# Optimization experiments

Hardware: AMD Instinct MI355X
Metric: run time of the kernel (lower is better)

The kernel has to match this reference:

```python
import jax, jax.numpy as jnp
import numpy as np

SAMPLERATE = 22050
N_OCTAVES = 16
N_SAMPLES = 2 ** 15  # 32768
N_EVENTS = 64
BATCH = 4
MIN_HZ = 20
MAX_HZ = 3000
BASE_RESONANCE = 0.01

MIN_FREQ = MIN_HZ / (SAMPLERATE // 2)
MAX_FREQ = MAX_HZ / (SAMPLERATE // 2)
FREQ_RANGE = MAX_FREQ - MIN_FREQ


def setup_inputs() -> dict:
    key = jax.random.key(0)
    k1, k2, k3, k4 = jax.random.split(key, 4)
    return {
        "f0": jax.random.uniform(k1, (BATCH, N_EVENTS, 1), dtype=jnp.float32),
        "decay_coefficients": jax.random.normal(k2, (BATCH, N_EVENTS, 1), dtype=jnp.float32),
        "phase_offsets": jax.random.normal(k3, (BATCH, N_EVENTS, 1), dtype=jnp.float32),
        "freq_spacing": jax.random.uniform(k4, (BATCH, N_EVENTS, 1), dtype=jnp.float32),
    }


def reference(f0, decay_coefficients, phase_offsets, freq_spacing):
    b, e, _ = f0.shape
    f0 = jnp.abs(f0)  # (B, E, 1)

    # computed in the original forward but never used in the output
    _ = jax.nn.sigmoid(phase_offsets) * np.pi

    # exponential_decay(torch.sigmoid(decay_coefficients), ...) -> double sigmoid
    dv = jax.nn.sigmoid(jax.nn.sigmoid(decay_coefficients))  # (B, E, 1)
    resonance_factor = (1.0 - BASE_RESONANCE) * 0.95
    decay = BASE_RESONANCE + dv * resonance_factor
    log_decay = jnp.log(decay + 1e-12)
    # cumsum of the constant over n_frames = n_octaves; F.interpolate to the
    # same size (n_samples=n_octaves in the call) is an identity.
    exp_decays = jnp.exp(jnp.cumsum(
        jnp.broadcast_to(log_decay, (b, e, N_OCTAVES)), axis=-1))  # (B, E, O)

    f0 = (MIN_FREQ + f0 * FREQ_RANGE) * np.pi  # (B, E, 1)
    factors = jnp.cumsum(
        jnp.broadcast_to(freq_spacing, (b, e, N_OCTAVES)), axis=-1)  # (B, E, O)
    f0s = f0 * factors  # (B, E, O) per-octave angular increments

    # cumulative phase over samples, then sin oscillator bank
    phase = jnp.cumsum(
        jnp.broadcast_to(f0s[..., None], (b, e, N_OCTAVES, N_SAMPLES)), axis=-1)
    osc = jnp.sin(phase) * exp_decays[..., None]  # (B, E, O, S)
    osc = jnp.sum(osc, axis=2)  # (B, E, S)

    # max_norm along the sample dim
    mx = jnp.max(jnp.abs(osc), axis=-1, keepdims=True)
    return osc / (mx + 1e-8)
```

## Files before the change

kernel.cpp:

```cpp
#include <hip/hip_runtime.h>
#include <math.h>

#pragma clang fp contract(off)

constexpr int NSAMP = 32768;
constexpr int NROWS = 256;
constexpr int NOCT  = 16;
constexpr int SEGS  = 16;
constexpr int TPB   = 256;
constexpr int GRID  = NROWS * SEGS;

__device__ __forceinline__ float keepf(float x) {
  asm volatile("" : "+v"(x));
  return x;
}

__global__ __launch_bounds__(TPB, 8) void f0res_k1(
    const float* __restrict__ f0_in,
    const float* __restrict__ dec_in,
    const float* __restrict__ fs_in,
    float* __restrict__ out,
    float* __restrict__ segmax)
{
  const int bid = blockIdx.x;
  const int row = bid >> 4;
  const int seg = bid & 15;
  const int t   = threadIdx.x;

  __shared__ float s_tab[NOCT][64];
  __shared__ float s_w[NOCT];
  __shared__ float s_carr[NOCT][128];
  __shared__ float s_red[TPB / 64];

  const float f0a = fabsf(f0_in[row]);
  const float dcc = dec_in[row];
  const float fsv = fs_in[row];

  const float MIN_F = (float)(20.0 / 11025.0);
  const float RNG_F = (float)(3000.0 / 11025.0 - 20.0 / 11025.0);
  const float c1s   = keepf(f0a * RNG_F);
  const float c2s   = keepf(MIN_F + c1s);
  const float f0ang = keepf(c2s * (float)M_PI);

  const float sg    = 1.0f / (1.0f + expf(-dcc));
  const float dvv   = 1.0f / (1.0f + expf(-sg));
  const float dvr   = keepf(dvv * 0.9405f);
  const float decay = keepf(0.01f + dvr);
  const float ldv   = logf(decay + 1e-12f);

  if (t < NOCT) {
    const int k = t;
    float fac = 0.0f;
    for (int j = 0; j <= k; ++j) fac = fac + fsv;
    const float x = keepf(f0ang * fac);
    float* tab = s_tab[k];
    float a = 0.0f;
#pragma unroll
    for (int i = 0; i < 16; ++i) { a = a + x;  tab[i]      = a; }
    const float T0 = a; a = 0.0f;
#pragma unroll
    for (int i = 0; i < 16; ++i) { a = a + T0; tab[16 + i] = a; }
    const float T1 = a; a = 0.0f;
#pragma unroll
    for (int i = 0; i < 16; ++i) { a = a + T1; tab[32 + i] = a; }
    const float T2 = a; a = 0.0f;
#pragma unroll
    for (int i = 0; i < 8;  ++i) { a = a + T2; tab[48 + i] = a; }
    float lc = 0.0f;
    for (int j = 0; j <= k; ++j) lc = lc + ldv;
    s_w[k] = expf(lc);
  }
  __syncthreads();

#pragma unroll
  for (int i = 0; i < (NOCT * 128) / TPB; ++i) {
    const int idx = t + i * TPB;
    const int k   = idx >> 7;
    const int lm  = idx & 127;
    const int m   = (seg << 7) + lm - 1;
    const float* tab = s_tab[k];
    float c = 0.0f;
    if (m >= 0) {
      c = tab[16 + (m & 15)];
      const int m2 = (m >> 4) - 1;
      if (m2 >= 0) {
        float p2 = tab[32 + (m2 & 15)];
        const int m3 = (m2 >> 4) - 1;
        if (m3 >= 0) p2 = p2 + tab[48 + m3];
        c = c + p2;
      }
    }
    s_carr[k][lm] = c;
  }
  __syncthreads();

  const double INV2PI_D = 0.15915494309189533577;
  const float I1 = (float)INV2PI_D;
  const float I2 = (float)(INV2PI_D - (double)I1);

  const int lm = t >> 1;
  const int a0base = (t & 1) * 2;

  float osc[8];
#pragma unroll
  for (int e = 0; e < 8; ++e) osc[e] = 0.0f;

#pragma unroll 2
  for (int k = 0; k < NOCT; ++k) {
    const float carry = s_carr[k][lm];
    const float w = s_w[k];

    float tv[8];
    *(float4*)&tv[0] = ((const float4*)s_tab[k])[a0base];
    *(float4*)&tv[4] = ((const float4*)s_tab[k])[a0base + 1];

#pragma unroll
    for (int e = 0; e < 8; ++e) {
      const float p  = tv[e] + carry;
      const float kq = rintf(p * I1);
      float fr = __builtin_fmaf(p, I1, -kq);
      fr = __builtin_fmaf(p, I2, fr);
      float sv;
      asm("v_sin_f32 %0, %1" : "=v"(sv) : "v"(fr));
      osc[e] = __builtin_fmaf(w, sv, osc[e]);
    }
  }

  float lmax = 0.0f;
#pragma unroll
  for (int e = 0; e < 8; ++e) lmax = fmaxf(lmax, fabsf(osc[e]));
#pragma unroll
  for (int off = 32; off >= 1; off >>= 1)
    lmax = fmaxf(lmax, __shfl_xor(lmax, off, 64));
  if ((t & 63) == 0) s_red[t >> 6] = lmax;
  __syncthreads();
  if (t == 0) {
    float mx = s_red[0];
#pragma unroll
    for (int i = 1; i < TPB / 64; ++i) mx = fmaxf(mx, s_red[i]);
    segmax[bid] = mx;
  }

  float4* o4 = (float4*)out + (size_t)bid * 512;
#pragma unroll
  for (int q = 0; q < 2; ++q) {
    float4 v;
    v.x = osc[4 * q + 0];
    v.y = osc[4 * q + 1];
    v.z = osc[4 * q + 2];
    v.w = osc[4 * q + 3];
    o4[q * 256 + t] = v;
  }
}

__global__ __launch_bounds__(TPB, 8) void f0res_k2(
    float* __restrict__ out,
    const float* __restrict__ segmax)
{
  const int bid = blockIdx.x;
  const int t   = threadIdx.x;
  const int row = bid >> 4;

  float mx = 0.0f;
#pragma unroll
  for (int i = 0; i < SEGS; ++i) mx = fmaxf(mx, segmax[row * SEGS + i]);
  const float inv = 1.0f / (mx + 1e-8f);

  float4* base = (float4*)out + (size_t)bid * 512;

  float4 v[2];
#pragma unroll
  for (int q = 0; q < 2; ++q) {
    const int s = (t & 1) * 256 + q * 128 + (t >> 1);
    v[q] = base[s];
  }
  __syncthreads();
#pragma unroll
  for (int q = 0; q < 2; ++q) {
    float4 x = v[q];
    x.x *= inv; x.y *= inv; x.z *= inv; x.w *= inv;
    base[q * 256 + t] = x;
  }
}

extern "C" void kernel_launch(void* const* d_in, const int* in_sizes, int n_in,
                              void* d_out, int out_size, void* d_ws, size_t ws_size,
                              hipStream_t stream) {
    const float* f0  = (const float*)d_in[0];
    const float* dcc = (const float*)d_in[1];
    const float* fsp = (const float*)d_in[3];
    float* out = (float*)d_out;
    float* segmax = (float*)d_ws;

    f0res_k1<<<GRID, TPB, 0, stream>>>(f0, dcc, fsp, out, segmax);
    f0res_k2<<<GRID, TPB, 0, stream>>>(out, segmax);
}
```

Measured before the change: 45.78 us.

## Replace per-sample sine with angle-addition from precomputed sin/cos tables

Precomputes sin and cos of each carry term and of the per-lane table phases in shared memory. The inner loop then builds sin(a+c) from the angle-addition identity plus a first-order correction for float rounding, instead of a range reduction and hardware sine per sample. This trades transcendental work for extra shared-memory loads and FMAs. Occupancy launch bounds drop from 8 to 6, and the substitution may change numerical accuracy relative to the rounded cumulative phase.

```diff
diff --git a/kernel.cpp b/kernel.cpp
--- a/kernel.cpp
+++ b/kernel.cpp
@@ -15,7 +15,14 @@
   return x;
 }
 
-__global__ __launch_bounds__(TPB, 8) void f0res_k1(
+__device__ __forceinline__ float hwsin(float fr) {
+  float s; asm("v_sin_f32 %0, %1" : "=v"(s) : "v"(fr)); return s;
+}
+__device__ __forceinline__ float hwcos(float fr) {
+  float c; asm("v_cos_f32 %0, %1" : "=v"(c) : "v"(fr)); return c;
+}
+
+__global__ __launch_bounds__(TPB, 6) void f0res_k1(
     const float* __restrict__ f0_in,
     const float* __restrict__ dec_in,
     const float* __restrict__ fs_in,
@@ -30,7 +37,15 @@
   __shared__ float s_tab[NOCT][64];
   __shared__ float s_w[NOCT];
   __shared__ float s_carr[NOCT][128];
+  __shared__ float s_cc[NOCT][128];
+  __shared__ float s_sc[NOCT][128];
+  __shared__ float s_sa[NOCT][16];
+  __shared__ float s_ca[NOCT][16];
   __shared__ float s_red[TPB / 64];
+
+  const double INV2PI_D = 0.15915494309189533577;
+  const float I1 = (float)INV2PI_D;
+  const float I2 = (float)(INV2PI_D - (double)I1);
 
   const float f0a = fabsf(f0_in[row]);
   const float dcc = dec_in[row];
@@ -91,12 +106,22 @@
       }
     }
     s_carr[k][lm] = c;
-  }
-  __syncthreads();
-
-  const double INV2PI_D = 0.15915494309189533577;
-  const float I1 = (float)INV2PI_D;
-  const float I2 = (float)(INV2PI_D - (double)I1);
+    const float kq = rintf(c * I1);
+    float fr = __builtin_fmaf(c, I1, -kq);
+    fr = __builtin_fmaf(c, I2, fr);
+    s_sc[k][lm] = hwsin(fr);
+    s_cc[k][lm] = hwcos(fr);
+  }
+  {
+    const int k = t >> 4, i = t & 15;
+    const float a0 = s_tab[k][i];
+    const float kq = rintf(a0 * I1);
+    float fr = __builtin_fmaf(a0, I1, -kq);
+    fr = __builtin_fmaf(a0, I2, fr);
+    s_sa[k][i] = hwsin(fr);
+    s_ca[k][i] = hwcos(fr);
+  }
+  __syncthreads();
 
   const int lm = t >> 1;
   const int a0base = (t & 1) * 2;
@@ -108,20 +133,29 @@
 #pragma unroll 2
   for (int k = 0; k < NOCT; ++k) {
     const float carry = s_carr[k][lm];
-    const float w = s_w[k];
-
-    float tv[8];
+    const float cC    = s_cc[k][lm];
+    const float sC    = s_sc[k][lm];
+    const float w     = s_w[k];
+
+    float tv[8], sa[8], ca[8];
     *(float4*)&tv[0] = ((const float4*)s_tab[k])[a0base];
     *(float4*)&tv[4] = ((const float4*)s_tab[k])[a0base + 1];
+    *(float4*)&sa[0] = ((const float4*)s_sa[k])[a0base & 3 ? a0base : a0base];
+    *(float4*)&sa[4] = ((const float4*)s_sa[k])[a0base + 1];
+    *(float4*)&ca[0] = ((const float4*)s_ca[k])[a0base];
+    *(float4*)&ca[4] = ((const float4*)s_ca[k])[a0base + 1];
+    *(float4*)&sa[0] = ((const float4*)s_sa[k])[a0base];
 
 #pragma unroll
     for (int e = 0; e < 8; ++e) {
       const float p  = tv[e] + carry;
-      const float kq = rintf(p * I1);
-      float fr = __builtin_fmaf(p, I1, -kq);
-      fr = __builtin_fmaf(p, I2, fr);
-      float sv;
-      asm("v_sin_f32 %0, %1" : "=v"(sv) : "v"(fr));
+      const float z  = p - carry;
+      const float ep = z - tv[e];
+      float t1 = sa[e] * cC;
+      t1 = __builtin_fmaf(ca[e], sC, t1);
+      float t2 = ca[e] * cC;
+      t2 = __builtin_fmaf(-sa[e], sC, t2);
+      const float sv = __builtin_fmaf(ep, t2, t1);
       osc[e] = __builtin_fmaf(w, sv, osc[e]);
     }
   }
```

New measurement: 51.34 us. 12.1% more time.
